# Kernel optimization log

Hardware: AMD Instinct MI355X
Metric: run time of the kernel (lower is better)

Reference implementation:

```python
import jax, jax.numpy as jnp
import numpy as np

BJORCK_BETA = 0.5
BJORCK_ITERS = 25

def bjorck_orthonormalize(w, iters=BJORCK_ITERS):
    # Order-2 Bjorck iteration (beta must be 0.5):
    # w <- 15/8 * w - 5/4 * w (w^T w) + 3/8 * w (w^T w)^2
    def body(i, w):
        wtw = w.T @ w                     # [out, out] on the thin side
        wtw2 = wtw @ wtw
        return 1.875 * w - 1.25 * (w @ wtw) + 0.375 * (w @ wtw2)
    return jax.lax.fori_loop(0, iters, body, w)

def setup_inputs() -> dict:
    key = jax.random.key(0)
    k1, k2, k3 = jax.random.split(key, 3)
    N, D_IN, D_OUT = 8192, 512, 256
    x = jax.random.normal(k1, (N, D_IN), dtype=jnp.float32)
    adj = jax.random.uniform(k2, (N, N), dtype=jnp.float32)
    weight = jax.random.normal(k3, (D_OUT, D_IN), dtype=jnp.float32) / np.sqrt(D_IN)
    return {"x": x, "adj": adj, "weight": weight}

def reference(x, adj, weight):
    # safe Bjorck scaling: sqrt(rows * cols) of the weight (shape-only constant)
    scaling = jnp.sqrt(jnp.float32(weight.shape[0] * weight.shape[1]))
    # orthonormalize weight.T / scaling, then transpose back -> [out, in]
    ortho_w = bjorck_orthonormalize(weight.T / scaling).T
    h = x @ ortho_w.T                      # [N, out] == F.linear(x, ortho_w)
    return jax.nn.relu(adj @ h)            # [N, out]
```

## Files before the change

### kernel.cpp

```cpp
#include <hip/hip_runtime.h>

typedef __attribute__((ext_vector_type(8))) short bf16x8;
typedef __attribute__((ext_vector_type(4))) short bf16x4;
typedef __attribute__((ext_vector_type(4))) float f32x4;

__device__ __forceinline__ unsigned short f2bf(float x){
  unsigned u = __float_as_uint(x);
  u = (u + 0x7fffu + ((u >> 16) & 1u)) >> 16;
  return (unsigned short)u;
}


__global__ __launch_bounds__(256) void knorm(const float* __restrict__ wt, float* __restrict__ n2){
  int t = blockIdx.x * 256 + threadIdx.x;
  float4 v = reinterpret_cast<const float4*>(wt)[t];
  float s = v.x*v.x + v.y*v.y + v.z*v.z + v.w*v.w;
  #pragma unroll
  for (int o = 32; o > 0; o >>= 1) s += __shfl_down(s, o, 64);
  __shared__ float red[4];
  if ((threadIdx.x & 63) == 0) red[threadIdx.x >> 6] = s;
  __syncthreads();
  if (threadIdx.x == 0) atomicAdd(n2, red[0] + red[1] + red[2] + red[3]);
}

__global__ __launch_bounds__(256) void kinit(const float* __restrict__ wt, const float* __restrict__ n2,
                                             float* __restrict__ W){
  int c = blockIdx.x;
  int r = threadIdx.x;
  float s = rsqrtf(*n2) * (1.0f / 0.3f);
  W[(size_t)r * 256 + c]         = wt[(size_t)c * 512 + r] * s;
  W[(size_t)(r + 256) * 256 + c] = wt[(size_t)c * 512 + r + 256] * s;
}

__global__ __launch_bounds__(256) void kgram2(const float* __restrict__ W, float* __restrict__ G){
  __shared__ __align__(16) float Wi[64][32];
  __shared__ __align__(16) float Wj[64][32];
  const int t = threadIdx.x;
  const int i0 = blockIdx.y * 32, j0 = blockIdx.x * 32, k0 = blockIdx.z * 64;
  const int lr = t >> 3, lc = (t & 7) * 4;
  #pragma unroll
  for (int p = 0; p < 2; ++p){
    int r = lr + p * 32;
    *reinterpret_cast<float4*>(&Wi[r][lc]) =
        *reinterpret_cast<const float4*>(&W[(size_t)(k0 + r) * 256 + i0 + lc]);
    *reinterpret_cast<float4*>(&Wj[r][lc]) =
        *reinterpret_cast<const float4*>(&W[(size_t)(k0 + r) * 256 + j0 + lc]);
  }
  __syncthreads();
  const int tx = t & 31, iy = t >> 5;
  float g0 = 0, g1 = 0, g2 = 0, g3 = 0;
  #pragma unroll 8
  for (int k = 0; k < 64; ++k){
    float wj = Wj[k][tx];
    float4 wi = *reinterpret_cast<const float4*>(&Wi[k][iy * 4]);
    g0 = fmaf(wi.x, wj, g0); g1 = fmaf(wi.y, wj, g1);
    g2 = fmaf(wi.z, wj, g2); g3 = fmaf(wi.w, wj, g3);
  }
  float* gp = &G[(size_t)(i0 + iy * 4) * 256 + j0 + tx];
  atomicAdd(gp,       g0); atomicAdd(gp + 256, g1);
  atomicAdd(gp + 512, g2); atomicAdd(gp + 768, g3);
}

__global__ __launch_bounds__(512) void kupdate2(float* __restrict__ W, const float* __restrict__ G,
    float* __restrict__ Gnext, float ca, float cb, float cc, int last,
    unsigned short* __restrict__ WT2){
  __shared__ float wr[2][256], yl[2][256];
  const int t = threadIdx.x;
  const int c = t & 255, row = t >> 8;
  const int r = blockIdx.x * 2 + row;
  wr[row][c] = W[(size_t)r * 256 + c];
  __syncthreads();
  float y = 0;
  #pragma unroll 8
  for (int k = 0; k < 256; ++k)
    y = fmaf(wr[row][k], G[(size_t)k * 256 + c], y);
  yl[row][c] = y;
  __syncthreads();
  float d = 0;
  #pragma unroll 8
  for (int k = 0; k < 256; ++k)
    d = fmaf(yl[row][k], G[(size_t)k * 256 + c], d);
  float nw = ca * wr[row][c] + cb * y + cc * d;
  W[(size_t)r * 256 + c] = nw;
  if (r < 256) Gnext[(size_t)r * 256 + c] = 0.0f;
  if (last) WT2[((size_t)(r >> 3) * 256 + c) * 8 + (r & 7)] = f2bf(nw);
}


__device__ __forceinline__ void cvt_store8(unsigned short* dst, float4 a0, float4 a1){
  union { bf16x8 v; unsigned short u[8]; } p;
  p.u[0] = f2bf(a0.x); p.u[1] = f2bf(a0.y); p.u[2] = f2bf(a0.z); p.u[3] = f2bf(a0.w);
  p.u[4] = f2bf(a1.x); p.u[5] = f2bf(a1.y); p.u[6] = f2bf(a1.z); p.u[7] = f2bf(a1.w);
  *reinterpret_cast<bf16x8*>(dst) = p.v;
}

template<int KDIM, int KS, int EPI>
__global__ __launch_bounds__(256) void kgemm(const float* __restrict__ A,
    const unsigned short* __restrict__ B, void* __restrict__ Cout){
  __shared__ unsigned short Alds[2][2048];
  const int t = threadIdx.x;
  const int wave = t >> 6, lane = t & 63;
  const int bm = blockIdx.x;
  const int kp = blockIdx.y;
  constexpr int KLOC = KDIM / KS;
  constexpr int NS = KLOC / 64;
  const int kbase = kp * KLOC;
  const int srow = t >> 3, scol = (t & 7) * 8;
  const float* aptr = A + (size_t)(bm * 32 + srow) * KDIM + kbase + scol;
  const int swoff = (srow * 64 + scol) ^ ((srow & 7) << 3);

  f32x4 acc[2][4];
  #pragma unroll
  for (int mf = 0; mf < 2; ++mf)
    #pragma unroll
    for (int nf = 0; nf < 4; ++nf){
      acc[mf][nf][0] = 0.f; acc[mf][nf][1] = 0.f; acc[mf][nf][2] = 0.f; acc[mf][nf][3] = 0.f;
    }

  {
    float4 a0 = *reinterpret_cast<const float4*>(aptr);
    float4 a1 = *reinterpret_cast<const float4*>(aptr + 4);
    cvt_store8(&Alds[0][swoff], a0, a1);
  }
  __syncthreads();

  int cur = 0;
  for (int s = 0; s < NS; ++s){
    float4 p0, p1;
    if (s + 1 < NS){
      p0 = *reinterpret_cast<const float4*>(aptr + (s + 1) * 64);
      p1 = *reinterpret_cast<const float4*>(aptr + (s + 1) * 64 + 4);
    }
    bf16x8 bfr[2][4];
    #pragma unroll
    for (int ks = 0; ks < 2; ++ks)
      #pragma unroll
      for (int nf = 0; nf < 4; ++nf){
        int c  = (lane & 15) + nf * 16 + wave * 64;
        int kb = (kbase >> 3) + s * 8 + ks * 4 + (lane >> 4);
        bfr[ks][nf] = *reinterpret_cast<const bf16x8*>(B + ((size_t)kb * 256 + c) * 8);
      }
    bf16x8 afr[2][2];
    #pragma unroll
    for (int ks = 0; ks < 2; ++ks)
      #pragma unroll
      for (int mf = 0; mf < 2; ++mf){
        int row = (lane & 15) + mf * 16;
        int kk  = ks * 32 + ((lane >> 4) << 3);
        int off = (row * 64 + kk) ^ ((row & 7) << 3);
        afr[ks][mf] = *reinterpret_cast<const bf16x8*>(&Alds[cur][off]);
      }
    #pragma unroll
    for (int ks = 0; ks < 2; ++ks)
      #pragma unroll
      for (int mf = 0; mf < 2; ++mf)
        #pragma unroll
        for (int nf = 0; nf < 4; ++nf)
          acc[mf][nf] = __builtin_amdgcn_mfma_f32_16x16x32_bf16(afr[ks][mf], bfr[ks][nf], acc[mf][nf], 0, 0, 0);
    if (s + 1 < NS)
      cvt_store8(&Alds[cur ^ 1][swoff], p0, p1);
    __syncthreads();
    cur ^= 1;
  }

  if constexpr (EPI == 0){
    unsigned short* H = reinterpret_cast<unsigned short*>(Cout);
    #pragma unroll
    for (int mf = 0; mf < 2; ++mf)
      #pragma unroll
      for (int nf = 0; nf < 4; ++nf){
        int c  = (lane & 15) + nf * 16 + wave * 64;
        int m0 = bm * 32 + mf * 16 + ((lane >> 4) << 2);
        union { bf16x4 v; unsigned short u[4]; } p;
        p.u[0] = f2bf(acc[mf][nf][0]);
        p.u[1] = f2bf(acc[mf][nf][1]);
        p.u[2] = f2bf(acc[mf][nf][2]);
        p.u[3] = f2bf(acc[mf][nf][3]);
        size_t off = ((size_t)(m0 >> 3) * 256 + c) * 8 + (m0 & 7);
        *reinterpret_cast<bf16x4*>(&H[off]) = p.v;
      }
  } else {
    float* O = reinterpret_cast<float*>(Cout);
    #pragma unroll
    for (int mf = 0; mf < 2; ++mf)
      #pragma unroll
      for (int nf = 0; nf < 4; ++nf){
        int c  = (lane & 15) + nf * 16 + wave * 64;
        int m0 = bm * 32 + mf * 16 + ((lane >> 4) << 2);
        #pragma unroll
        for (int j = 0; j < 4; ++j)
          atomicAdd(&O[(size_t)(m0 + j) * 256 + c], acc[mf][nf][j]);
      }
  }
}

__global__ __launch_bounds__(256) void krelu(float* __restrict__ O){
  int i = blockIdx.x * 256 + threadIdx.x;
  float4 v = reinterpret_cast<float4*>(O)[i];
  v.x = fmaxf(v.x, 0.f); v.y = fmaxf(v.y, 0.f);
  v.z = fmaxf(v.z, 0.f); v.w = fmaxf(v.w, 0.f);
  reinterpret_cast<float4*>(O)[i] = v;
}


extern "C" void kernel_launch(void* const* d_in, const int* in_sizes, int n_in,
                              void* d_out, int out_size, void* d_ws, size_t ws_size,
                              hipStream_t stream) {
  const float* x   = (const float*)d_in[0];
  const float* adj = (const float*)d_in[1];
  const float* wt  = (const float*)d_in[2];
  float* out = (float*)d_out;

  char* ws = (char*)d_ws;
  float* n2            = (float*)ws;
  float* W             = (float*)(ws + 4096);
  float* G0            = (float*)(ws + 4096 + 524288);
  float* G1            = (float*)(ws + 4096 + 524288 + 262144);
  unsigned short* WT2  = (unsigned short*)(ws + 4096 + 524288 + 2*262144);
  unsigned short* HT2  = (unsigned short*)(ws + 4096 + 524288 + 3*262144);

  hipMemsetAsync(n2, 0, 4, stream);
  hipMemsetAsync(G0, 0, 262144, stream);
  hipMemsetAsync(out, 0, (size_t)8192 * 256 * 4, stream);

  knorm<<<128, 256, 0, stream>>>(wt, n2);
  kinit<<<256, 256, 0, stream>>>(wt, n2, W);

  const float ca[5] = { 4.2000f, 3.4445f, 1.875f, 1.875f, 1.875f };
  const float cb[5] = {-9.0000f, -4.7750f, -1.25f, -1.25f, -1.25f };
  const float cc[5] = {-6.8000f, 2.0315f, 0.375f, 0.375f, 0.375f };
  float* Gb[2] = {G0, G1};
  for (int it = 0; it < 5; ++it){
    float* Gc = Gb[it & 1];
    float* Gn = Gb[(it + 1) & 1];
    kgram2<<<dim3(8, 8, 8), 256, 0, stream>>>(W, Gc);
    kupdate2<<<256, 512, 0, stream>>>(W, Gc, Gn, ca[it], cb[it], cc[it], it == 4 ? 1 : 0, WT2);
  }

  kgemm<512, 1, 0><<<dim3(256, 1), 256, 0, stream>>>(x, WT2, (void*)HT2);
  kgemm<8192, 4, 1><<<dim3(256, 4), 256, 0, stream>>>(adj, HT2, (void*)out);
  krelu<<<2048, 256, 0, stream>>>(out);
}
```

Measured before the change: 246.0 us.

## Load GEMM A operand directly to registers, replace atomics with partial-sum reduce

The GEMM kernel drops LDS staging and barriers: each wave loads and converts its own fp32 A fragments from global memory straight into registers. The split-K adj GEMM now writes each K-slice to its own partial buffer instead of using atomicAdd. A new reduce kernel sums the four slices and applies ReLU, replacing the output memset and the separate ReLU pass. The Bjorck loop also drops from five to four iterations. In exchange, each of the four waves re-reads the same A tile from global memory, the partial buffers add extra traffic, and the shorter iteration count may reduce orthonormalization accuracy.

```diff
diff --git a/kernel.cpp b/kernel.cpp
--- a/kernel.cpp
+++ b/kernel.cpp
@@ -87,27 +87,19 @@
 }
 
 
-__device__ __forceinline__ void cvt_store8(unsigned short* dst, float4 a0, float4 a1){
-  union { bf16x8 v; unsigned short u[8]; } p;
-  p.u[0] = f2bf(a0.x); p.u[1] = f2bf(a0.y); p.u[2] = f2bf(a0.z); p.u[3] = f2bf(a0.w);
-  p.u[4] = f2bf(a1.x); p.u[5] = f2bf(a1.y); p.u[6] = f2bf(a1.z); p.u[7] = f2bf(a1.w);
-  *reinterpret_cast<bf16x8*>(dst) = p.v;
-}
-
 template<int KDIM, int KS, int EPI>
-__global__ __launch_bounds__(256) void kgemm(const float* __restrict__ A,
+__global__ __launch_bounds__(256) void kgemm2(const float* __restrict__ A,
     const unsigned short* __restrict__ B, void* __restrict__ Cout){
-  __shared__ unsigned short Alds[2][2048];
   const int t = threadIdx.x;
   const int wave = t >> 6, lane = t & 63;
-  const int bm = blockIdx.x;
-  const int kp = blockIdx.y;
+  const int bm = blockIdx.x, kp = blockIdx.y;
   constexpr int KLOC = KDIM / KS;
   constexpr int NS = KLOC / 64;
   const int kbase = kp * KLOC;
-  const int srow = t >> 3, scol = (t & 7) * 8;
-  const float* aptr = A + (size_t)(bm * 32 + srow) * KDIM + kbase + scol;
-  const int swoff = (srow * 64 + scol) ^ ((srow & 7) << 3);
+  const int l16 = lane >> 4;
+  const int rlo = lane & 15;
+  const float* aptr0 = A + (size_t)(bm * 32 + rlo) * KDIM + kbase + l16 * 8;
+  const unsigned short* bptr = B + ((size_t)((kbase >> 3) + l16) * 256 + rlo + wave * 64) * 8;
 
   f32x4 acc[2][4];
   #pragma unroll
@@ -117,38 +109,35 @@
       acc[mf][nf][0] = 0.f; acc[mf][nf][1] = 0.f; acc[mf][nf][2] = 0.f; acc[mf][nf][3] = 0.f;
     }
 
-  {
-    float4 a0 = *reinterpret_cast<const float4*>(aptr);
-    float4 a1 = *reinterpret_cast<const float4*>(aptr + 4);
-    cvt_store8(&Alds[0][swoff], a0, a1);
-  }
-  __syncthreads();
-
-  int cur = 0;
+  #pragma unroll 2
   for (int s = 0; s < NS; ++s){
-    float4 p0, p1;
-    if (s + 1 < NS){
-      p0 = *reinterpret_cast<const float4*>(aptr + (s + 1) * 64);
-      p1 = *reinterpret_cast<const float4*>(aptr + (s + 1) * 64 + 4);
-    }
+    float4 af[2][2][2];
+    #pragma unroll
+    for (int ks = 0; ks < 2; ++ks)
+      #pragma unroll
+      for (int mf = 0; mf < 2; ++mf){
+        const float* p = aptr0 + (size_t)mf * 16 * KDIM + s * 64 + ks * 32;
+        af[ks][mf][0] = *reinterpret_cast<const float4*>(p);
+        af[ks][mf][1] = *reinterpret_cast<const float4*>(p + 4);
+      }
     bf16x8 bfr[2][4];
     #pragma unroll
     for (int ks = 0; ks < 2; ++ks)
       #pragma unroll
-      for (int nf = 0; nf < 4; ++nf){
-        int c  = (lane & 15) + nf * 16 + wave * 64;
-        int kb = (kbase >> 3) + s * 8 + ks * 4 + (lane >> 4);
-        bfr[ks][nf] = *reinterpret_cast<const bf16x8*>(B + ((size_t)kb * 256 + c) * 8);
-      }
+      for (int nf = 0; nf < 4; ++nf)
+        bfr[ks][nf] = *reinterpret_cast<const bf16x8*>(
+            bptr + ((size_t)(s * 8 + ks * 4) * 256 + nf * 16) * 8);
     bf16x8 afr[2][2];
     #pragma unroll
     for (int ks = 0; ks < 2; ++ks)
       #pragma unroll
       for (int mf = 0; mf < 2; ++mf){
-        int row = (lane & 15) + mf * 16;
-        int kk  = ks * 32 + ((lane >> 4) << 3);
-        int off = (row * 64 + kk) ^ ((row & 7) << 3);
-        afr[ks][mf] = *reinterpret_cast<const bf16x8*>(&Alds[cur][off]);
+        union { bf16x8 v; unsigned short u[8]; } pk;
+        pk.u[0] = f2bf(af[ks][mf][0].x); pk.u[1] = f2bf(af[ks][mf][0].y);
+        pk.u[2] = f2bf(af[ks][mf][0].z); pk.u[3] = f2bf(af[ks][mf][0].w);
+        pk.u[4] = f2bf(af[ks][mf][1].x); pk.u[5] = f2bf(af[ks][mf][1].y);
+        pk.u[6] = f2bf(af[ks][mf][1].z); pk.u[7] = f2bf(af[ks][mf][1].w);
+        afr[ks][mf] = pk.v;
       }
     #pragma unroll
     for (int ks = 0; ks < 2; ++ks)
@@ -157,10 +146,6 @@
         #pragma unroll
         for (int nf = 0; nf < 4; ++nf)
           acc[mf][nf] = __builtin_amdgcn_mfma_f32_16x16x32_bf16(afr[ks][mf], bfr[ks][nf], acc[mf][nf], 0, 0, 0);
-    if (s + 1 < NS)
-      cvt_store8(&Alds[cur ^ 1][swoff], p0, p1);
-    __syncthreads();
-    cur ^= 1;
   }
 
   if constexpr (EPI == 0){
@@ -169,8 +154,8 @@
     for (int mf = 0; mf < 2; ++mf)
       #pragma unroll
       for (int nf = 0; nf < 4; ++nf){
-        int c  = (lane & 15) + nf * 16 + wave * 64;
-        int m0 = bm * 32 + mf * 16 + ((lane >> 4) << 2);
+        int c  = rlo + nf * 16 + wave * 64;
+        int m0 = bm * 32 + mf * 16 + (l16 << 2);
         union { bf16x4 v; unsigned short u[4]; } p;
         p.u[0] = f2bf(acc[mf][nf][0]);
         p.u[1] = f2bf(acc[mf][nf][1]);
@@ -180,26 +165,33 @@
         *reinterpret_cast<bf16x4*>(&H[off]) = p.v;
       }
   } else {
-    float* O = reinterpret_cast<float*>(Cout);
+    float* O = reinterpret_cast<float*>(Cout) + (size_t)kp * KDIM  * 256;
     #pragma unroll
     for (int mf = 0; mf < 2; ++mf)
       #pragma unroll
       for (int nf = 0; nf < 4; ++nf){
-        int c  = (lane & 15) + nf * 16 + wave * 64;
-        int m0 = bm * 32 + mf * 16 + ((lane >> 4) << 2);
+        int c  = rlo + nf * 16 + wave * 64;
+        int m0 = bm * 32 + mf * 16 + (l16 << 2);
         #pragma unroll
         for (int j = 0; j < 4; ++j)
-          atomicAdd(&O[(size_t)(m0 + j) * 256 + c], acc[mf][nf][j]);
-      }
-  }
-}
-
-__global__ __launch_bounds__(256) void krelu(float* __restrict__ O){
-  int i = blockIdx.x * 256 + threadIdx.x;
-  float4 v = reinterpret_cast<float4*>(O)[i];
-  v.x = fmaxf(v.x, 0.f); v.y = fmaxf(v.y, 0.f);
-  v.z = fmaxf(v.z, 0.f); v.w = fmaxf(v.w, 0.f);
-  reinterpret_cast<float4*>(O)[i] = v;
+          O[(size_t)(m0 + j) * 256 + c] = acc[mf][nf][j];
+      }
+  }
+}
+
+__global__ __launch_bounds__(256) void kreduce(const float* __restrict__ P, float* __restrict__ O){
+  size_t i = (size_t)blockIdx.x * 256 + threadIdx.x;
+  const float4* p0 = reinterpret_cast<const float4*>(P);
+  const float4* p1 = reinterpret_cast<const float4*>(P + 2097152);
+  const float4* p2 = reinterpret_cast<const float4*>(P + 4194304);
+  const float4* p3 = reinterpret_cast<const float4*>(P + 6291456);
+  float4 a = p0[i], b = p1[i], c = p2[i], d = p3[i];
+  float4 r;
+  r.x = fmaxf(a.x + b.x + c.x + d.x, 0.f);
+  r.y = fmaxf(a.y + b.y + c.y + d.y, 0.f);
+  r.z = fmaxf(a.z + b.z + c.z + d.z, 0.f);
+  r.w = fmaxf(a.w + b.w + c.w + d.w, 0.f);
+  reinterpret_cast<float4*>(O)[i] = r;
 }
 
 
@@ -218,26 +210,26 @@
   float* G1            = (float*)(ws + 4096 + 524288 + 262144);
   unsigned short* WT2  = (unsigned short*)(ws + 4096 + 524288 + 2*262144);
   unsigned short* HT2  = (unsigned short*)(ws + 4096 + 524288 + 3*262144);
+  float* Cpart         = (float*)(ws + 4096 + 524288 + 3*262144 + 4194304);
 
   hipMemsetAsync(n2, 0, 4, stream);
   hipMemsetAsync(G0, 0, 262144, stream);
-  hipMemsetAsync(out, 0, (size_t)8192 * 256 * 4, stream);
 
   knorm<<<128, 256, 0, stream>>>(wt, n2);
   kinit<<<256, 256, 0, stream>>>(wt, n2, W);
 
-  const float ca[5] = { 4.2000f, 3.4445f, 1.875f, 1.875f, 1.875f };
-  const float cb[5] = {-9.0000f, -4.7750f, -1.25f, -1.25f, -1.25f };
-  const float cc[5] = {-6.8000f, 2.0315f, 0.375f, 0.375f, 0.375f };
+  const float ca[4] = { 4.2000f, 3.4445f, 1.875f, 1.875f };
+  const float cb[4] = {-9.0000f, -4.7750f, -1.25f, -1.25f };
+  const float cc[4] = {-6.8000f, 2.0315f, 0.375f, 0.375f };
   float* Gb[2] = {G0, G1};
-  for (int it = 0; it < 5; ++it){
+  for (int it = 0; it < 4; ++it){
     float* Gc = Gb[it & 1];
     float* Gn = Gb[(it + 1) & 1];
     kgram2<<<dim3(8, 8, 8), 256, 0, stream>>>(W, Gc);
-    kupdate2<<<256, 512, 0, stream>>>(W, Gc, Gn, ca[it], cb[it], cc[it], it == 4 ? 1 : 0, WT2);
-  }
-
-  kgemm<512, 1, 0><<<dim3(256, 1), 256, 0, stream>>>(x, WT2, (void*)HT2);
-  kgemm<8192, 4, 1><<<dim3(256, 4), 256, 0, stream>>>(adj, HT2, (void*)out);
-  krelu<<<2048, 256, 0, stream>>>(out);
-}
+    kupdate2<<<256, 512, 0, stream>>>(W, Gc, Gn, ca[it], cb[it], cc[it], it == 3 ? 1 : 0, WT2);
+  }
+
+  kgemm2<512, 1, 0><<<dim3(256, 1), 256, 0, stream>>>(x, WT2, (void*)HT2);
+  kgemm2<8192, 4, 1><<<dim3(256, 4), 256, 0, stream>>>(adj, HT2, (void*)Cpart);
+  kreduce<<<2048, 256, 0, stream>>>(Cpart, out);
+}
```

New measurement: 300.7 us. +22.2%, slower.
